# Kernel tuning notes

Hardware: AMD Instinct MI355X
Metric: run time of the kernel (lower is better)

## Reference

```python
import jax, jax.numpy as jnp
import numpy as np

# dims: batch, seq, d_model, d_hidden, routed experts, top-k, shared experts
B, S, D, H, E_R, K, E_S = 2, 1024, 1024, 512, 64, 6, 2
EPS = 1.1920929e-07  # torch.finfo(float32).eps, RMSNorm default when eps=None


def setup_inputs() -> dict:
    key = jax.random.key(0)
    ks = jax.random.split(key, 8)
    u = lambda k, shape, b: jax.random.uniform(k, shape, jnp.float32, -b, b)
    bd = 1.0 / np.sqrt(D)   # bound for W1 (1/sqrt(d_input)) and W2 (1/sqrt(d_output)=1/sqrt(D))
    bh = 1.0 / np.sqrt(H)
    return {
        "x": jax.random.normal(ks[0], (B, S, D), jnp.float32),
        "norm_w": jnp.ones((D,), jnp.float32),            # RMSNorm weight
        "Wr": u(ks[1], (E_R, D), bd),                      # router Linear weight (no bias)
        "sW1": u(ks[2], (E_S, D, H), bd), "sb1": jnp.zeros((E_S, 1, H), jnp.float32),
        "sW2": u(ks[3], (E_S, H, D), bd), "sb2": jnp.zeros((E_S, 1, D), jnp.float32),
        "sWg": u(ks[4], (H, H), bh),                       # shared-experts SwiGLU gate weight
        "rW1": u(ks[5], (E_R, D, H), bd), "rb1": jnp.zeros((E_R, 1, H), jnp.float32),
        "rW2": u(ks[6], (E_R, H, D), bd), "rb2": jnp.zeros((E_R, 1, D), jnp.float32),
        "rWg": u(ks[7], (H, H), bh),                       # routed-experts SwiGLU gate weight
        "bias": jnp.full((E_R,), 1.0 / E_R, jnp.float32), # routing bias buffer (expert_bias=True)
    }


def _rmsnorm(x, w):
    ms = jnp.mean(x * x, axis=-1, keepdims=True)
    return x * jax.lax.rsqrt(ms + EPS) * w


def _swiglu(h, Wg):
    # SwiGLU(d_model=H): silu(h @ Wg) * h, elementwise gate over hidden dim
    return jax.nn.silu(h @ Wg) * h


def reference(x, norm_w, Wr, sW1, sb1, sW2, sb2, sWg, rW1, rb1, rW2, rb2, rWg, bias):
    xn = _rmsnorm(x, norm_w)
    t = xn.reshape(-1, D)                                  # (T, D) tokens
    # --- shared experts, summed over expert axis ---
    hs = jnp.einsum('td,edh->teh', t, sW1) + sb1[None, :, 0, :]
    hs = _swiglu(hs, sWg)
    shared = jnp.einsum('teh,ehd->td', hs, sW2) + jnp.sum(sb2[:, 0, :], axis=0)
    # --- router ---
    raw = t @ Wr.T                                         # (T, E_R) raw affinity
    aff = jax.lax.stop_gradient(raw) + bias                # detached + bias for top-k selection
    _, idx = jax.lax.top_k(aff, K)                         # (T, K)
    # --- routed experts: dense all-expert FFN, gather top-k outputs ---
    # (mathematically identical to the source's per-token weight gather,
    #  but avoids materializing (T,K,D,H) weight tensors)
    h = jnp.einsum('td,edh->teh', t, rW1) + rb1[None, :, 0, :]   # (T, E_R, H)
    h = _swiglu(h, rWg)
    out_all = jnp.einsum('teh,ehd->ted', h, rW2) + rb2[None, :, 0, :]  # (T, E_R, D)
    out_k = jnp.take_along_axis(out_all, idx[:, :, None], axis=1)      # (T, K, D)
    aff_k = jnp.take_along_axis(raw, idx, axis=1)                      # (T, K) raw (undetached)
    w = aff_k / jnp.sum(aff_k, axis=-1, keepdims=True)                 # expert_bias=True path
    routed = jnp.einsum('tk,tkd->td', w, out_k)                        # (T, D)
    return x + (shared + routed).reshape(B, S, D)
```

## Files before the change

kernel.cpp:

```cpp
#include <hip/hip_runtime.h>
#include <cstdint>
#include <cstddef>

typedef unsigned short u16;
typedef unsigned int u32;
typedef __attribute__((ext_vector_type(8))) short bh8;
typedef __attribute__((ext_vector_type(4))) float fx4;

#define T_TOK 2048
#define D_DIM 1024
#define H_DIM 512
#define N_EXP 64
#define K_TOP 6
#define N_ASG (T_TOK * K_TOP)
#define R_TOT (N_ASG + 2 * T_TOK)
#define GRID_E (8 * 9 * 64)

__device__ __forceinline__ float bf2f(u16 v) {
    union { u32 u; float f; } c; c.u = ((u32)v) << 16; return c.f;
}
__device__ __forceinline__ u16 f2bf(float f) {
    union { u32 u; float f; } c; c.f = f;
    u32 u = c.u;
    return (u16)((u + 0x7fffu + ((u >> 16) & 1u)) >> 16);
}

__global__ __launch_bounds__(256) void rn4_k(
    const float* __restrict__ x, const float* __restrict__ nw,
    const float* __restrict__ Wr, float* __restrict__ raw, u16* __restrict__ xnb)
{
    int t0 = blockIdx.x << 2, tid = threadIdx.x;
    __shared__ float xs[4][D_DIM];
    __shared__ float ps[4][256];
    __shared__ float red4[4][4];
    int d0 = tid << 2;
    float4 wv = *(const float4*)(nw + d0);
    float4 xv[4];
    #pragma unroll
    for (int tt = 0; tt < 4; ++tt) {
        xv[tt] = *(const float4*)(x + (size_t)(t0 + tt) * D_DIM + d0);
        float ss = xv[tt].x * xv[tt].x + xv[tt].y * xv[tt].y
                 + xv[tt].z * xv[tt].z + xv[tt].w * xv[tt].w;
        #pragma unroll
        for (int o = 32; o > 0; o >>= 1) ss += __shfl_down(ss, o);
        if ((tid & 63) == 0) red4[tt][tid >> 6] = ss;
    }
    __syncthreads();
    #pragma unroll
    for (int tt = 0; tt < 4; ++tt) {
        float ms = (red4[tt][0] + red4[tt][1] + red4[tt][2] + red4[tt][3]) * (1.f / (float)D_DIM);
        float sc = rsqrtf(ms + 1.1920929e-07f);
        float4 xf;
        xf.x = xv[tt].x * sc * wv.x;
        xf.y = xv[tt].y * sc * wv.y;
        xf.z = xv[tt].z * sc * wv.z;
        xf.w = xv[tt].w * sc * wv.w;
        *(float4*)&xs[tt][d0] = xf;
        ushort4 ob;
        ob.x = f2bf(xf.x); ob.y = f2bf(xf.y); ob.z = f2bf(xf.z); ob.w = f2bf(xf.w);
        *(ushort4*)(xnb + (size_t)(t0 + tt) * D_DIM + d0) = ob;
    }
    __syncthreads();
    int e = tid & 63, part = tid >> 6;
    const float* wr = Wr + (size_t)e * D_DIM + part * 256;
    float s0 = 0.f, s1 = 0.f, s2 = 0.f, s3 = 0.f;
    const float* xp0 = &xs[0][part * 256];
    const float* xp1 = &xs[1][part * 256];
    const float* xp2 = &xs[2][part * 256];
    const float* xp3 = &xs[3][part * 256];
    #pragma unroll 4
    for (int i = 0; i < 256; i += 4) {
        float4 w4 = *(const float4*)(wr + i);
        s0 += xp0[i] * w4.x + xp0[i+1] * w4.y + xp0[i+2] * w4.z + xp0[i+3] * w4.w;
        s1 += xp1[i] * w4.x + xp1[i+1] * w4.y + xp1[i+2] * w4.z + xp1[i+3] * w4.w;
        s2 += xp2[i] * w4.x + xp2[i+1] * w4.y + xp2[i+2] * w4.z + xp2[i+3] * w4.w;
        s3 += xp3[i] * w4.x + xp3[i+1] * w4.y + xp3[i+2] * w4.z + xp3[i+3] * w4.w;
    }
    ps[0][tid] = s0; ps[1][tid] = s1; ps[2][tid] = s2; ps[3][tid] = s3;
    __syncthreads();
    if (part == 0) {
        #pragma unroll
        for (int tt = 0; tt < 4; ++tt)
            raw[(size_t)(t0 + tt) * N_EXP + e] =
                ps[tt][e] + ps[tt][64 + e] + ps[tt][128 + e] + ps[tt][192 + e];
    }
}

__global__ void topk_k(const float* __restrict__ raw, const float* __restrict__ ebias,
                       int* __restrict__ cnt, int* __restrict__ tki, float* __restrict__ tkw)
{
    int t = blockIdx.x, lane = threadIdx.x;
    float r = raw[(size_t)t * N_EXP + lane];
    float cur = r + ebias[lane];
    int selI[K_TOP]; float selR[K_TOP];
    #pragma unroll
    for (int k = 0; k < K_TOP; ++k) {
        float v = cur; int id = lane;
        #pragma unroll
        for (int o = 32; o > 0; o >>= 1) {
            float v2 = __shfl_down(v, o); int i2 = __shfl_down(id, o);
            if (v2 > v || (v2 == v && i2 < id)) { v = v2; id = i2; }
        }
        id = __shfl(id, 0);
        if (lane == id) cur = -3.4e38f;
        selI[k] = id;
        selR[k] = __shfl(r, id);
    }
    float s = 0.f;
    #pragma unroll
    for (int k = 0; k < K_TOP; ++k) s += selR[k];
    if (lane < K_TOP) {
        tki[t * K_TOP + lane] = selI[lane];
        tkw[t * K_TOP + lane] = selR[lane] / s;
        atomicAdd(&cnt[selI[lane]], 1);
    }
}

__global__ void scan_k(const int* __restrict__ cnt, int* __restrict__ offs, int* __restrict__ fill)
{
    int lane = threadIdx.x;
    int c = cnt[lane];
    int s = c;
    #pragma unroll
    for (int o = 1; o < 64; o <<= 1) {
        int v = __shfl_up(s, o);
        if (lane >= o) s += v;
    }
    int excl = s - c;
    offs[lane] = excl;
    fill[lane] = excl;
    if (lane == 63) offs[N_EXP] = s;
}

__global__ void fill_k(const int* __restrict__ tki, const float* __restrict__ tkw,
                       int* __restrict__ fill, int* __restrict__ atok, float* __restrict__ aw,
                       int* __restrict__ rowOf)
{
    int t = blockIdx.x, lane = threadIdx.x;
    if (lane < K_TOP) {
        int e = tki[t * K_TOP + lane];
        int p = atomicAdd(&fill[e], 1);
        atok[p] = t;
        aw[p] = tkw[t * K_TOP + lane];
        rowOf[t * K_TOP + lane] = p;
    }
}

__global__ __launch_bounds__(256) void convAll_k(
    const float* __restrict__ rW1, const float* __restrict__ sW1,
    const float* __restrict__ rW2, const float* __restrict__ sW2,
    const float* __restrict__ rWg, const float* __restrict__ sWg,
    u16* __restrict__ W1f, u16* __restrict__ W2f, u16* __restrict__ Wgf)
{
    int id = blockIdx.x;
    const float* src; u16* dst;
    int K, N, n0, k0;
    const size_t MS = (size_t)H_DIM * D_DIM;
    if (id < 66 * 128) {
        int mat = id >> 7, tile = id & 127;
        K = D_DIM; N = H_DIM;
        src = (mat < N_EXP ? rW1 + (size_t)mat * MS : sW1 + (size_t)(mat - N_EXP) * MS);
        dst = W1f + (size_t)mat * MS;
        n0 = (tile & 7) << 6; k0 = (tile >> 3) << 6;
    } else if (id < 2 * 66 * 128) {
        id -= 66 * 128;
        int mat = id >> 7, tile = id & 127;
        K = H_DIM; N = D_DIM;
        src = (mat < N_EXP ? rW2 + (size_t)mat * MS : sW2 + (size_t)(mat - N_EXP) * MS);
        dst = W2f + (size_t)mat * MS;
        n0 = (tile & 15) << 6; k0 = (tile >> 4) << 6;
    } else {
        id -= 2 * 66 * 128;
        int mat = id >> 6, tile = id & 63;
        K = H_DIM; N = H_DIM;
        src = (mat == 0 ? rWg : sWg);
        dst = Wgf + (size_t)mat * (H_DIM * H_DIM);
        n0 = (tile & 7) << 6; k0 = (tile >> 3) << 6;
    }

    __shared__ u16 t[64][68];
    int tid = threadIdx.x;
    int kr = tid >> 4, c4 = (tid & 15) << 2;
    #pragma unroll
    for (int rr = 0; rr < 4; ++rr) {
        int k = (rr << 4) + kr;
        float4 v = *(const float4*)(src + (size_t)(k0 + k) * N + n0 + c4);
        t[c4 + 0][k] = f2bf(v.x);
        t[c4 + 1][k] = f2bf(v.y);
        t[c4 + 2][k] = f2bf(v.z);
        t[c4 + 3][k] = f2bf(v.w);
    }
    __syncthreads();
    int lane = tid & 63, g = tid >> 6;
    int nr = lane & 15, kq = lane >> 4;
    #pragma unroll
    for (int f = 0; f < 2; ++f) {
        int fragId = g + (f << 2);
        int ntile = fragId >> 1, kb = fragId & 1;
        bh8 v = *(const bh8*)&t[(ntile << 4) + nr][(kb << 5) + (kq << 3)];
        size_t fi = (((size_t)((n0 >> 4) + ntile) * (size_t)(K >> 5)
                      + (size_t)((k0 >> 5) + kb)) << 9) + (size_t)(lane << 3);
        *(bh8*)(dst + fi) = v;
    }
}

__device__ __forceinline__ bool slabDecode(
    int bx, const int* __restrict__ offs,
    int& e, int& rowBase, int& rows, int& tokBase)
{
    int xcd = bx & 7, rest = bx >> 3, grp = rest >> 6, slab = rest & 63;
    if (grp < 8) {
        e = (grp << 3) + xcd;
        int s0 = offs[e], s1 = offs[e + 1];
        rowBase = s0 + (slab << 5);
        if (rowBase >= s1) return false;
        rows = s1 - rowBase; if (rows > 32) rows = 32;
        tokBase = -1;
        return true;
    }
    int f = (slab << 3) + xcd;
    if (f >= 128) return false;
    int sh = f & 1;
    e = N_EXP + sh;
    tokBase = (f >> 1) << 5;
    rowBase = N_ASG + (sh << 11) + tokBase;
    rows = 32;
    return true;
}

__global__ __launch_bounds__(256, 4) void p1_k(
    const u16* __restrict__ xnb, const u16* __restrict__ W1f,
    const float* __restrict__ rb1, const float* __restrict__ sb1,
    const int* __restrict__ offs, const int* __restrict__ atok,
    u16* __restrict__ h)
{
    int e, rowBase, rows, tokBase;
    if (!slabDecode(blockIdx.x, offs, e, rowBase, rows, tokBase)) return;

    __shared__ int tok[32];
    int tid = threadIdx.x;
    if (tid < 32) {
        int cl = tid < rows ? tid : rows - 1;
        tok[tid] = (tokBase < 0) ? atok[rowBase + cl] : tokBase + tid;
    }
    __syncthreads();

    int w = tid >> 6, lane = tid & 63, quad = lane >> 4, l15 = lane & 15;
    int cg = blockIdx.y;
    int nt0 = (cg << 4) + (w << 2);
    const u16* bp = W1f + (size_t)e * (H_DIM * D_DIM)
                  + (((size_t)nt0 << 5) << 9) + (lane << 3);
    const u16* a0p = xnb + (size_t)tok[l15] * D_DIM + (quad << 3);
    const u16* a1p = xnb + (size_t)tok[16 + l15] * D_DIM + (quad << 3);
    const float* b1 = (tokBase < 0) ? rb1 + e * H_DIM : sb1 + (e - N_EXP) * H_DIM;

    fx4 ac0[4] = {}, ac1[4] = {};
    bh8 bA[4], bB[4], aA0, aA1, aB0, aB1;
    #pragma unroll
    for (int ct = 0; ct < 4; ++ct) bA[ct] = *(const bh8*)(bp + ((size_t)(ct << 5) << 9));
    aA0 = *(const bh8*)a0p; aA1 = *(const bh8*)a1p;
    #pragma unroll 1
    for (int kb = 0; kb < 32; kb += 2) {
        #pragma unroll
        for (int ct = 0; ct < 4; ++ct) bB[ct] = *(const bh8*)(bp + (((ct << 5) + kb + 1) << 9));
        aB0 = *(const bh8*)(a0p + ((kb + 1) << 5));
        aB1 = *(const bh8*)(a1p + ((kb + 1) << 5));
        #pragma unroll
        for (int ct = 0; ct < 4; ++ct) {
            ac0[ct] = __builtin_amdgcn_mfma_f32_16x16x32_bf16(aA0, bA[ct], ac0[ct], 0, 0, 0);
            ac1[ct] = __builtin_amdgcn_mfma_f32_16x16x32_bf16(aA1, bA[ct], ac1[ct], 0, 0, 0);
        }
        #pragma unroll
        for (int ct = 0; ct < 4; ++ct) bA[ct] = *(const bh8*)(bp + (((ct << 5) + kb + 2) << 9));
        aA0 = *(const bh8*)(a0p + ((kb + 2) << 5));
        aA1 = *(const bh8*)(a1p + ((kb + 2) << 5));
        #pragma unroll
        for (int ct = 0; ct < 4; ++ct) {
            ac0[ct] = __builtin_amdgcn_mfma_f32_16x16x32_bf16(aB0, bB[ct], ac0[ct], 0, 0, 0);
            ac1[ct] = __builtin_amdgcn_mfma_f32_16x16x32_bf16(aB1, bB[ct], ac1[ct], 0, 0, 0);
        }
    }
    #pragma unroll
    for (int ct = 0; ct < 4; ++ct) {
        int col = ((nt0 + ct) << 4) + l15;
        float bv = b1[col];
        #pragma unroll
        for (int r = 0; r < 4; ++r) {
            int r0 = (quad << 2) + r;
            if (r0 < rows) h[(size_t)(rowBase + r0) * H_DIM + col] = f2bf(ac0[ct][r] + bv);
            int r1 = 16 + r0;
            if (r1 < rows) h[(size_t)(rowBase + r1) * H_DIM + col] = f2bf(ac1[ct][r] + bv);
        }
    }
}

__global__ __launch_bounds__(256, 4) void p2_k(
    u16* __restrict__ h, const u16* __restrict__ Wgf)
{
    int rowBase = blockIdx.x << 4;
    int tid = threadIdx.x;
    int w = tid >> 6, lane = tid & 63, quad = lane >> 4, l15 = lane & 15;
    const u16* bp = Wgf + (rowBase < N_ASG ? 0 : (size_t)(H_DIM * H_DIM)) + (lane << 3);
    const u16* a0p = h + (size_t)(rowBase + l15) * H_DIM + (quad << 3);

    fx4 ac[8] = {};
    bh8 bA[8], bB[8], aA, aB;
    #pragma unroll
    for (int ct = 0; ct < 8; ++ct)
        bA[ct] = *(const bh8*)(bp + ((((size_t)(w << 3) + ct) << 4) << 9));
    aA = *(const bh8*)a0p;
    #pragma unroll 1
    for (int kb = 0; kb < 16; kb += 2) {
        #pragma unroll
        for (int ct = 0; ct < 8; ++ct)
            bB[ct] = *(const bh8*)(bp + (((((size_t)(w << 3) + ct) << 4) + kb + 1) << 9));
        aB = *(const bh8*)(a0p + ((kb + 1) << 5));
        #pragma unroll
        for (int ct = 0; ct < 8; ++ct)
            ac[ct] = __builtin_amdgcn_mfma_f32_16x16x32_bf16(aA, bA[ct], ac[ct], 0, 0, 0);
        #pragma unroll
        for (int ct = 0; ct < 8; ++ct)
            bA[ct] = *(const bh8*)(bp + (((((size_t)(w << 3) + ct) << 4) + kb + 2) << 9));
        aA = *(const bh8*)(a0p + ((kb + 2) << 5));
        #pragma unroll
        for (int ct = 0; ct < 8; ++ct)
            ac[ct] = __builtin_amdgcn_mfma_f32_16x16x32_bf16(aB, bB[ct], ac[ct], 0, 0, 0);
    }
    __syncthreads();
    #pragma unroll
    for (int ct = 0; ct < 8; ++ct) {
        int col = (((w << 3) + ct) << 4) + l15;
        #pragma unroll
        for (int r = 0; r < 4; ++r) {
            int row = rowBase + (quad << 2) + r;
            size_t i = (size_t)row * H_DIM + col;
            float g = ac[ct][r], hv = bf2f(h[i]);
            h[i] = f2bf(hv * g * (1.f / (1.f + __expf(-g))));
        }
    }
}

template<int ATOM>
__global__ __launch_bounds__(256, 4) void p3_k(
    const u16* __restrict__ hg, const u16* __restrict__ W2f,
    const float* __restrict__ rb2, const float* __restrict__ sb2,
    const int* __restrict__ offs, const int* __restrict__ atok,
    const float* __restrict__ aw, float* __restrict__ accG, float* __restrict__ outAll)
{
    int e, rowBase, rows, tokBase;
    if (!slabDecode(blockIdx.x, offs, e, rowBase, rows, tokBase)) return;

    __shared__ int tok[32];
    __shared__ float wt[32];
    int tid = threadIdx.x;
    if (tid < 32) {
        int cl = tid < rows ? tid : rows - 1;
        if (tokBase < 0) { tok[tid] = atok[rowBase + cl]; wt[tid] = aw[rowBase + cl]; }
        else             { tok[tid] = tokBase + tid;      wt[tid] = 1.0f; }
    }
    __syncthreads();

    int w = tid >> 6, lane = tid & 63, quad = lane >> 4, l15 = lane & 15;
    int cg = blockIdx.y;
    int nt0 = (cg << 4) + (w << 2);
    const u16* bp = W2f + (size_t)e * (H_DIM * D_DIM)
                  + (((size_t)nt0 << 4) << 9) + (lane << 3);
    const u16* a0p = hg + (size_t)(rowBase + l15) * H_DIM + (quad << 3);
    const u16* a1p = hg + (size_t)(rowBase + 16 + l15) * H_DIM + (quad << 3);
    const float* b2 = (tokBase < 0) ? rb2 + e * D_DIM : sb2 + (e - N_EXP) * D_DIM;

    fx4 ac0[4] = {}, ac1[4] = {};
    bh8 bA[4], bB[4], aA0, aA1, aB0, aB1;
    #pragma unroll
    for (int ct = 0; ct < 4; ++ct) bA[ct] = *(const bh8*)(bp + ((size_t)(ct << 4) << 9));
    aA0 = *(const bh8*)a0p; aA1 = *(const bh8*)a1p;
    #pragma unroll 1
    for (int kb = 0; kb < 16; kb += 2) {
        #pragma unroll
        for (int ct = 0; ct < 4; ++ct) bB[ct] = *(const bh8*)(bp + (((ct << 4) + kb + 1) << 9));
        aB0 = *(const bh8*)(a0p + ((kb + 1) << 5));
        aB1 = *(const bh8*)(a1p + ((kb + 1) << 5));
        #pragma unroll
        for (int ct = 0; ct < 4; ++ct) {
            ac0[ct] = __builtin_amdgcn_mfma_f32_16x16x32_bf16(aA0, bA[ct], ac0[ct], 0, 0, 0);
            ac1[ct] = __builtin_amdgcn_mfma_f32_16x16x32_bf16(aA1, bA[ct], ac1[ct], 0, 0, 0);
        }
        #pragma unroll
        for (int ct = 0; ct < 4; ++ct) bA[ct] = *(const bh8*)(bp + (((ct << 4) + kb + 2) << 9));
        aA0 = *(const bh8*)(a0p + ((kb + 2) << 5));
        aA1 = *(const bh8*)(a1p + ((kb + 2) << 5));
        #pragma unroll
        for (int ct = 0; ct < 4; ++ct) {
            ac0[ct] = __builtin_amdgcn_mfma_f32_16x16x32_bf16(aB0, bB[ct], ac0[ct], 0, 0, 0);
            ac1[ct] = __builtin_amdgcn_mfma_f32_16x16x32_bf16(aB1, bB[ct], ac1[ct], 0, 0, 0);
        }
    }
    #pragma unroll
    for (int ct = 0; ct < 4; ++ct) {
        int col = ((nt0 + ct) << 4) + l15;
        float bv = b2[col];
        #pragma unroll
        for (int r = 0; r < 4; ++r) {
            int r0 = (quad << 2) + r;
            if (r0 < rows) {
                float v = wt[r0] * (ac0[ct][r] + bv);
                if (ATOM) atomicAdd(&accG[(size_t)tok[r0] * D_DIM + col], v);
                else      outAll[(size_t)(rowBase + r0) * D_DIM + col] = v;
            }
            int r1 = 16 + r0;
            if (r1 < rows) {
                float v = wt[r1] * (ac1[ct][r] + bv);
                if (ATOM) atomicAdd(&accG[(size_t)tok[r1] * D_DIM + col], v);
                else      outAll[(size_t)(rowBase + r1) * D_DIM + col] = v;
            }
        }
    }
}

__global__ __launch_bounds__(256) void gather_k(
    const float* __restrict__ x, const float* __restrict__ outAll,
    const int* __restrict__ rowOf, float* __restrict__ out)
{
    int t = blockIdx.x, tid = threadIdx.x;
    __shared__ int rws[K_TOP];
    if (tid < K_TOP) rws[tid] = rowOf[t * K_TOP + tid];
    __syncthreads();
    int d0 = tid << 2;
    size_t base = (size_t)t * D_DIM + d0;
    float4 xv = *(const float4*)(x + base);
    float4 s = *(const float4*)(outAll + (size_t)(N_ASG + t) * D_DIM + d0);
    float4 s1 = *(const float4*)(outAll + (size_t)(N_ASG + T_TOK + t) * D_DIM + d0);
    s.x += s1.x; s.y += s1.y; s.z += s1.z; s.w += s1.w;
    #pragma unroll
    for (int k = 0; k < K_TOP; ++k) {
        float4 v = *(const float4*)(outAll + (size_t)rws[k] * D_DIM + d0);
        s.x += v.x; s.y += v.y; s.z += v.z; s.w += v.w;
    }
    float4 o;
    o.x = xv.x + s.x; o.y = xv.y + s.y; o.z = xv.z + s.z; o.w = xv.w + s.w;
    *(float4*)(out + base) = o;
}

template<int ROUTED>
__global__ __launch_bounds__(256) void moe_ffn_k(
    const u16* __restrict__ xnb,
    const float* __restrict__ W1b, const float* __restrict__ Wg,
    const float* __restrict__ W2b,
    const float* __restrict__ b1b, const float* __restrict__ b2b,
    const int* __restrict__ offs, const int* __restrict__ atok,
    const float* __restrict__ aw, float* __restrict__ accG)
{
    int e = blockIdx.z;
    int start = ROUTED ? offs[e] : 0;
    int end   = ROUTED ? offs[e + 1] : T_TOK;
    int rowBase = start + (blockIdx.y << 5);
    if (rowBase >= end) return;
    int rows = end - rowBase; if (rows > 32) rows = 32;

    __shared__ int   tok[32];
    __shared__ float wt[32];
    __shared__ u16 hA[32 * 520];
    __shared__ u16 hG[32 * 520];
    __shared__ u16 As[32 * 32];
    __shared__ u16 Bs[64 * 36];

    int tid = threadIdx.x;
    if (tid < 32) {
        int cl = rowBase + tid; if (cl >= end) cl = end - 1;
        tok[tid] = ROUTED ? atok[cl] : cl;
        wt[tid]  = ROUTED ? aw[cl] : 1.0f;
    }
    __syncthreads();

    const float* W1 = W1b + (size_t)e * (D_DIM * H_DIM);
    const float* W2 = W2b + (size_t)e * (D_DIM * H_DIM);
    const float* b1 = b1b + e * H_DIM;
    const float* b2 = b2b + e * D_DIM;

    int w = tid >> 6, lane = tid & 63, quad = lane >> 4, l15 = lane & 15;
    int sr2 = tid >> 3, sc2 = (tid & 7) << 2;

    for (int nc = 0; nc < 8; ++nc) {
        int n0 = nc << 6;
        fx4 a0 = {}; fx4 a1 = {};
        for (int kc = 0; kc < 32; ++kc) {
            int kb = kc << 5;
            int2 av = *(const int2*)(xnb + (size_t)tok[sr2] * D_DIM + kb + sc2);
            const float* cp = W1 + n0 + lane;
            int kx = kb + (w << 3);
            u32 p[4];
            #pragma unroll
            for (int jj = 0; jj < 4; ++jj) {
                u32 lo = f2bf(cp[(size_t)(kx + 2 * jj) * H_DIM]);
                u32 hi = f2bf(cp[(size_t)(kx + 2 * jj + 1) * H_DIM]);
                p[jj] = lo | (hi << 16);
            }
            __syncthreads();
            *(int2*)&As[sr2 * 32 + sc2] = av;
            u16* bsw = &Bs[lane * 36 + (w << 3)];
            uint2 q0; q0.x = p[0]; q0.y = p[1];
            uint2 q1; q1.x = p[2]; q1.y = p[3];
            *(uint2*)bsw = q0;
            *(uint2*)(bsw + 4) = q1;
            __syncthreads();
            bh8 af0 = *(const bh8*)&As[l15 * 32 + (quad << 3)];
            bh8 af1 = *(const bh8*)&As[(16 + l15) * 32 + (quad << 3)];
            const u16* brp = &Bs[((w << 4) + l15) * 36 + (quad << 3)];
            union { bh8 v; uint2 u2[2]; } bf;
            bf.u2[0] = *(const uint2*)brp;
            bf.u2[1] = *(const uint2*)(brp + 4);
            a0 = __builtin_amdgcn_mfma_f32_16x16x32_bf16(af0, bf.v, a0, 0, 0, 0);
            a1 = __builtin_amdgcn_mfma_f32_16x16x32_bf16(af1, bf.v, a1, 0, 0, 0);
        }
        int col = n0 + (w << 4) + l15;
        float bv = b1[col];
        #pragma unroll
        for (int r = 0; r < 4; ++r) {
            hA[((quad << 2) + r) * 520 + col]      = f2bf(a0[r] + bv);
            hA[(16 + (quad << 2) + r) * 520 + col] = f2bf(a1[r] + bv);
        }
    }
    __syncthreads();

    for (int nc = 0; nc < 8; ++nc) {
        int n0 = nc << 6;
        fx4 a0 = {}; fx4 a1 = {};
        for (int kc = 0; kc < 16; ++kc) {
            int kb = kc << 5;
            const float* cp = Wg + n0 + lane;
            int kx = kb + (w << 3);
            u32 p[4];
            #pragma unroll
            for (int jj = 0; jj < 4; ++jj) {
                u32 lo = f2bf(cp[(size_t)(kx + 2 * jj) * H_DIM]);
                u32 hi = f2bf(cp[(size_t)(kx + 2 * jj + 1) * H_DIM]);
                p[jj] = lo | (hi << 16);
            }
            __syncthreads();
            u16* bsw = &Bs[lane * 36 + (w << 3)];
            uint2 q0; q0.x = p[0]; q0.y = p[1];
            uint2 q1; q1.x = p[2]; q1.y = p[3];
            *(uint2*)bsw = q0;
            *(uint2*)(bsw + 4) = q1;
            __syncthreads();
            bh8 af0 = *(const bh8*)&hA[l15 * 520 + kb + (quad << 3)];
            bh8 af1 = *(const bh8*)&hA[(16 + l15) * 520 + kb + (quad << 3)];
            const u16* brp = &Bs[((w << 4) + l15) * 36 + (quad << 3)];
            union { bh8 v; uint2 u2[2]; } bf;
            bf.u2[0] = *(const uint2*)brp;
            bf.u2[1] = *(const uint2*)(brp + 4);
            a0 = __builtin_amdgcn_mfma_f32_16x16x32_bf16(af0, bf.v, a0, 0, 0, 0);
            a1 = __builtin_amdgcn_mfma_f32_16x16x32_bf16(af1, bf.v, a1, 0, 0, 0);
        }
        int col = n0 + (w << 4) + l15;
        #pragma unroll
        for (int r = 0; r < 4; ++r) {
            int r0 = (quad << 2) + r;
            float h0 = bf2f(hA[r0 * 520 + col]);
            float g0 = a0[r];
            hG[r0 * 520 + col] = f2bf(h0 * g0 * (1.f / (1.f + __expf(-g0))));
            int r1 = 16 + r0;
            float h1 = bf2f(hA[r1 * 520 + col]);
            float g1 = a1[r];
            hG[r1 * 520 + col] = f2bf(h1 * g1 * (1.f / (1.f + __expf(-g1))));
        }
    }
    __syncthreads();

    for (int nc = 0; nc < 16; ++nc) {
        int n0 = nc << 6;
        fx4 a0 = {}; fx4 a1 = {};
        for (int kc = 0; kc < 16; ++kc) {
            int kb = kc << 5;
            const float* cp = W2 + n0 + lane;
            int kx = kb + (w << 3);
            u32 p[4];
            #pragma unroll
            for (int jj = 0; jj < 4; ++jj) {
                u32 lo = f2bf(cp[(size_t)(kx + 2 * jj) * D_DIM]);
                u32 hi = f2bf(cp[(size_t)(kx + 2 * jj + 1) * D_DIM]);
                p[jj] = lo | (hi << 16);
            }
            __syncthreads();
            u16* bsw = &Bs[lane * 36 + (w << 3)];
            uint2 q0; q0.x = p[0]; q0.y = p[1];
            uint2 q1; q1.x = p[2]; q1.y = p[3];
            *(uint2*)bsw = q0;
            *(uint2*)(bsw + 4) = q1;
            __syncthreads();
            bh8 af0 = *(const bh8*)&hG[l15 * 520 + kb + (quad << 3)];
            bh8 af1 = *(const bh8*)&hG[(16 + l15) * 520 + kb + (quad << 3)];
            const u16* brp = &Bs[((w << 4) + l15) * 36 + (quad << 3)];
            union { bh8 v; uint2 u2[2]; } bf;
            bf.u2[0] = *(const uint2*)brp;
            bf.u2[1] = *(const uint2*)(brp + 4);
            a0 = __builtin_amdgcn_mfma_f32_16x16x32_bf16(af0, bf.v, a0, 0, 0, 0);
            a1 = __builtin_amdgcn_mfma_f32_16x16x32_bf16(af1, bf.v, a1, 0, 0, 0);
        }
        int col = n0 + (w << 4) + l15;
        float bv = b2[col];
        #pragma unroll
        for (int r = 0; r < 4; ++r) {
            int lr0 = (quad << 2) + r;
            if (lr0 < rows)
                atomicAdd(&accG[(size_t)tok[lr0] * D_DIM + col], wt[lr0] * (a0[r] + bv));
            int lr1 = 16 + lr0;
            if (lr1 < rows)
                atomicAdd(&accG[(size_t)tok[lr1] * D_DIM + col], wt[lr1] * (a1[r] + bv));
        }
    }
}

__global__ __launch_bounds__(256) void final_k(
    const float* __restrict__ x, const float* __restrict__ acc, float* __restrict__ out)
{
    size_t i = ((size_t)blockIdx.x * 256 + threadIdx.x) << 2;
    float4 xv = *(const float4*)(x + i);
    float4 a = *(const float4*)(acc + i);
    float4 o;
    o.x = xv.x + a.x;
    o.y = xv.y + a.y;
    o.z = xv.z + a.z;
    o.w = xv.w + a.w;
    *(float4*)(out + i) = o;
}

extern "C" void kernel_launch(void* const* d_in, const int* in_sizes, int n_in,
                              void* d_out, int out_size, void* d_ws, size_t ws_size,
                              hipStream_t stream)
{
    const float* x     = (const float*)d_in[0];
    const float* nw    = (const float*)d_in[1];
    const float* Wr    = (const float*)d_in[2];
    const float* sW1   = (const float*)d_in[3];
    const float* sb1   = (const float*)d_in[4];
    const float* sW2   = (const float*)d_in[5];
    const float* sb2   = (const float*)d_in[6];
    const float* sWg   = (const float*)d_in[7];
    const float* rW1   = (const float*)d_in[8];
    const float* rb1   = (const float*)d_in[9];
    const float* rW2   = (const float*)d_in[10];
    const float* rb2   = (const float*)d_in[11];
    const float* rWg   = (const float*)d_in[12];
    const float* ebias = (const float*)d_in[13];
    float* out = (float*)d_out;
    (void)in_sizes; (void)n_in; (void)out_size;

    char* wp = (char*)d_ws;
    auto alloc = [&](size_t b) { char* p = wp; wp += (b + 255) & ~(size_t)255; return p; };
    int*   cnt  = (int*)alloc(N_EXP * 4);
    int*   offs = (int*)alloc((N_EXP + 1) * 4);
    int*   fill = (int*)alloc(N_EXP * 4);
    int*   tki  = (int*)alloc((size_t)T_TOK * K_TOP * 4);
    float* tkw  = (float*)alloc((size_t)T_TOK * K_TOP * 4);
    int*   atok = (int*)alloc((size_t)N_ASG * 4);
    float* aw   = (float*)alloc((size_t)N_ASG * 4);
    int*   rowOf= (int*)alloc((size_t)T_TOK * K_TOP * 4);
    float* raw  = (float*)alloc((size_t)T_TOK * N_EXP * 4);
    u16*   xnb  = (u16*)alloc((size_t)T_TOK * D_DIM * 2);
    float* acc  = (float*)alloc((size_t)T_TOK * D_DIM * 4);
    u16* W1f = (u16*)alloc((size_t)(N_EXP + 2) * H_DIM * D_DIM * 2);
    u16* W2f = (u16*)alloc((size_t)(N_EXP + 2) * H_DIM * D_DIM * 2);
    u16* Wgf = (u16*)alloc((size_t)2 * H_DIM * H_DIM * 2);
    u16* h   = (u16*)alloc((size_t)R_TOT * H_DIM * 2);
    alloc(1 << 16);
    char* markA = wp;
    float* outAll = (float*)alloc((size_t)R_TOT * D_DIM * 4);
    char* markB = wp;
    bool fastA = (size_t)(markA - (char*)d_ws) <= ws_size;
    bool fast2 = (size_t)(markB - (char*)d_ws) <= ws_size;

    hipMemsetAsync(cnt, 0, N_EXP * 4, stream);

    dim3 b256(256);
    rn4_k<<<T_TOK / 4, b256, 0, stream>>>(x, nw, Wr, raw, xnb);
    topk_k<<<T_TOK, dim3(64), 0, stream>>>(raw, ebias, cnt, tki, tkw);
    scan_k<<<1, dim3(64), 0, stream>>>(cnt, offs, fill);
    fill_k<<<T_TOK, dim3(64), 0, stream>>>(tki, tkw, fill, atok, aw, rowOf);

    if (fast2) {
        convAll_k<<<dim3(2 * 66 * 128 + 2 * 64), b256, 0, stream>>>(
            rW1, sW1, rW2, sW2, rWg, sWg, W1f, W2f, Wgf);
        p1_k<<<dim3(GRID_E, 2), b256, 0, stream>>>(xnb, W1f, rb1, sb1, offs, atok, h);
        p2_k<<<dim3(R_TOT / 16), b256, 0, stream>>>(h, Wgf);
        p3_k<0><<<dim3(GRID_E, 4), b256, 0, stream>>>(
            h, W2f, rb2, sb2, offs, atok, aw, nullptr, outAll);
        gather_k<<<T_TOK, b256, 0, stream>>>(x, outAll, rowOf, out);
    } else if (fastA) {
        hipMemsetAsync(acc, 0, (size_t)T_TOK * D_DIM * 4, stream);
        convAll_k<<<dim3(2 * 66 * 128 + 2 * 64), b256, 0, stream>>>(
            rW1, sW1, rW2, sW2, rWg, sWg, W1f, W2f, Wgf);
        p1_k<<<dim3(GRID_E, 2), b256, 0, stream>>>(xnb, W1f, rb1, sb1, offs, atok, h);
        p2_k<<<dim3(R_TOT / 16), b256, 0, stream>>>(h, Wgf);
        p3_k<1><<<dim3(GRID_E, 4), b256, 0, stream>>>(
            h, W2f, rb2, sb2, offs, atok, aw, acc, nullptr);
        final_k<<<(T_TOK * D_DIM) / 1024, b256, 0, stream>>>(x, acc, out);
    } else {
        hipMemsetAsync(acc, 0, (size_t)T_TOK * D_DIM * 4, stream);
        moe_ffn_k<1><<<dim3(1, 64, N_EXP), b256, 0, stream>>>(
            xnb, rW1, rWg, rW2, rb1, rb2, offs, atok, aw, acc);
        moe_ffn_k<0><<<dim3(1, 64, 2), b256, 0, stream>>>(
            xnb, sW1, sWg, sW2, sb1, sb2, offs, atok, aw, acc);
        final_k<<<(T_TOK * D_DIM) / 1024, b256, 0, stream>>>(x, acc, out);
    }
}
```

Baseline: 638.6 us.

## Fuse weight conversion into prep kernel and stage GEMM epilogues through LDS

Merges the bf16 weight-conversion pass into the RMSNorm/router kernel so both run in a single launch, with each conversion block now covering two 64-row k-slabs and prefetching the second slab while the first is written out. The p1 and p3 (non-atomic) epilogues now stage results in shared memory and write them to global memory as contiguous 16-byte row segments, replacing scattered per-element stores. This is meant to cut launch overhead and uncoalesced write traffic. In exchange it uses more LDS per block, which may lower occupancy, and adds an extra barrier in the epilogues.

```diff
diff --git a/kernel.cpp b/kernel.cpp
--- a/kernel.cpp
+++ b/kernel.cpp
@@ -15,6 +15,7 @@
 #define N_ASG (T_TOK * K_TOP)
 #define R_TOT (N_ASG + 2 * T_TOK)
 #define GRID_E (8 * 9 * 64)
+#define NCONV (66 * 64 + 66 * 64 + 64)
 
 __device__ __forceinline__ float bf2f(u16 v) {
     union { u32 u; float f; } c; c.u = ((u32)v) << 16; return c.f;
@@ -25,49 +26,134 @@
     return (u16)((u + 0x7fffu + ((u >> 16) & 1u)) >> 16);
 }
 
-__global__ __launch_bounds__(256) void rn4_k(
+__global__ __launch_bounds__(256) void prep_k(
     const float* __restrict__ x, const float* __restrict__ nw,
-    const float* __restrict__ Wr, float* __restrict__ raw, u16* __restrict__ xnb)
-{
-    int t0 = blockIdx.x << 2, tid = threadIdx.x;
-    __shared__ float xs[4][D_DIM];
-    __shared__ float ps[4][256];
-    __shared__ float red4[4][4];
+    const float* __restrict__ Wr, float* __restrict__ raw, u16* __restrict__ xnb,
+    const float* __restrict__ rW1, const float* __restrict__ sW1,
+    const float* __restrict__ rW2, const float* __restrict__ sW2,
+    const float* __restrict__ rWg, const float* __restrict__ sWg,
+    u16* __restrict__ W1f, u16* __restrict__ W2f, u16* __restrict__ Wgf,
+    int nconv)
+{
+    __shared__ __align__(16) char smraw[20608];
+    int id = blockIdx.x;
+    int tid = threadIdx.x;
+
+    if (id < nconv) {
+        const size_t MS = (size_t)H_DIM * D_DIM;
+        const float* src; u16* dst;
+        int K, N, n0, k0;
+        if (id < 4224) {
+            int mat = id >> 6, j = id & 63;
+            K = D_DIM; N = H_DIM;
+            src = (mat < N_EXP ? rW1 + (size_t)mat * MS : sW1 + (size_t)(mat - N_EXP) * MS);
+            dst = W1f + (size_t)mat * MS;
+            n0 = (j & 7) << 6; k0 = (j >> 3) << 7;
+        } else if (id < 8448) {
+            int t = id - 4224, mat = t >> 6, j = t & 63;
+            K = H_DIM; N = D_DIM;
+            src = (mat < N_EXP ? rW2 + (size_t)mat * MS : sW2 + (size_t)(mat - N_EXP) * MS);
+            dst = W2f + (size_t)mat * MS;
+            n0 = (j & 15) << 6; k0 = (j >> 4) << 7;
+        } else {
+            int t = id - 8448, mat = t >> 5, j = t & 31;
+            K = H_DIM; N = H_DIM;
+            src = (mat == 0 ? rWg : sWg);
+            dst = Wgf + (size_t)mat * (H_DIM * H_DIM);
+            n0 = (j & 7) << 6; k0 = (j >> 3) << 7;
+        }
+        u16 (*t0)[68] = reinterpret_cast<u16(*)[68]>(smraw);
+        u16 (*t1)[68] = reinterpret_cast<u16(*)[68]>(smraw + 8704);
+        int kr = tid >> 4, c4 = (tid & 15) << 2;
+        int lane = tid & 63, g = tid >> 6, nr = lane & 15, kq = lane >> 4;
+
+        float4 v[4];
+        #pragma unroll
+        for (int rr = 0; rr < 4; ++rr)
+            v[rr] = *(const float4*)(src + (size_t)(k0 + (rr << 4) + kr) * N + n0 + c4);
+        #pragma unroll
+        for (int rr = 0; rr < 4; ++rr) {
+            int k = (rr << 4) + kr;
+            t0[c4 + 0][k] = f2bf(v[rr].x);
+            t0[c4 + 1][k] = f2bf(v[rr].y);
+            t0[c4 + 2][k] = f2bf(v[rr].z);
+            t0[c4 + 3][k] = f2bf(v[rr].w);
+        }
+        __syncthreads();
+        float4 w4_[4];
+        #pragma unroll
+        for (int rr = 0; rr < 4; ++rr)
+            w4_[rr] = *(const float4*)(src + (size_t)(k0 + 64 + (rr << 4) + kr) * N + n0 + c4);
+        #pragma unroll
+        for (int f = 0; f < 2; ++f) {
+            int fragId = g + (f << 2);
+            int ntile = fragId >> 1, kb2 = fragId & 1;
+            bh8 vv = *(const bh8*)&t0[(ntile << 4) + nr][(kb2 << 5) + (kq << 3)];
+            size_t fi = (((size_t)((n0 >> 4) + ntile) * (size_t)(K >> 5)
+                          + (size_t)((k0 >> 5) + kb2)) << 9) + (size_t)(lane << 3);
+            *(bh8*)(dst + fi) = vv;
+        }
+        #pragma unroll
+        for (int rr = 0; rr < 4; ++rr) {
+            int k = (rr << 4) + kr;
+            t1[c4 + 0][k] = f2bf(w4_[rr].x);
+            t1[c4 + 1][k] = f2bf(w4_[rr].y);
+            t1[c4 + 2][k] = f2bf(w4_[rr].z);
+            t1[c4 + 3][k] = f2bf(w4_[rr].w);
+        }
+        __syncthreads();
+        #pragma unroll
+        for (int f = 0; f < 2; ++f) {
+            int fragId = g + (f << 2);
+            int ntile = fragId >> 1, kb2 = fragId & 1;
+            bh8 vv = *(const bh8*)&t1[(ntile << 4) + nr][(kb2 << 5) + (kq << 3)];
+            size_t fi = (((size_t)((n0 >> 4) + ntile) * (size_t)(K >> 5)
+                          + (size_t)((k0 >> 5) + 2 + kb2)) << 9) + (size_t)(lane << 3);
+            *(bh8*)(dst + fi) = vv;
+        }
+        return;
+    }
+
+    int t0tok = (id - nconv) << 2;
+    float* xs = (float*)smraw;
+    float* ps = xs + 4 * D_DIM;
+    float* red4 = ps + 4 * 256;
     int d0 = tid << 2;
     float4 wv = *(const float4*)(nw + d0);
     float4 xv[4];
     #pragma unroll
     for (int tt = 0; tt < 4; ++tt) {
-        xv[tt] = *(const float4*)(x + (size_t)(t0 + tt) * D_DIM + d0);
+        xv[tt] = *(const float4*)(x + (size_t)(t0tok + tt) * D_DIM + d0);
         float ss = xv[tt].x * xv[tt].x + xv[tt].y * xv[tt].y
                  + xv[tt].z * xv[tt].z + xv[tt].w * xv[tt].w;
         #pragma unroll
         for (int o = 32; o > 0; o >>= 1) ss += __shfl_down(ss, o);
-        if ((tid & 63) == 0) red4[tt][tid >> 6] = ss;
+        if ((tid & 63) == 0) red4[tt * 4 + (tid >> 6)] = ss;
     }
     __syncthreads();
     #pragma unroll
     for (int tt = 0; tt < 4; ++tt) {
-        float ms = (red4[tt][0] + red4[tt][1] + red4[tt][2] + red4[tt][3]) * (1.f / (float)D_DIM);
+        float ms = (red4[tt * 4 + 0] + red4[tt * 4 + 1] + red4[tt * 4 + 2] + red4[tt * 4 + 3])
+                 * (1.f / (float)D_DIM);
         float sc = rsqrtf(ms + 1.1920929e-07f);
         float4 xf;
         xf.x = xv[tt].x * sc * wv.x;
         xf.y = xv[tt].y * sc * wv.y;
         xf.z = xv[tt].z * sc * wv.z;
         xf.w = xv[tt].w * sc * wv.w;
-        *(float4*)&xs[tt][d0] = xf;
+        *(float4*)&xs[tt * D_DIM + d0] = xf;
         ushort4 ob;
         ob.x = f2bf(xf.x); ob.y = f2bf(xf.y); ob.z = f2bf(xf.z); ob.w = f2bf(xf.w);
-        *(ushort4*)(xnb + (size_t)(t0 + tt) * D_DIM + d0) = ob;
+        *(ushort4*)(xnb + (size_t)(t0tok + tt) * D_DIM + d0) = ob;
     }
     __syncthreads();
     int e = tid & 63, part = tid >> 6;
     const float* wr = Wr + (size_t)e * D_DIM + part * 256;
     float s0 = 0.f, s1 = 0.f, s2 = 0.f, s3 = 0.f;
-    const float* xp0 = &xs[0][part * 256];
-    const float* xp1 = &xs[1][part * 256];
-    const float* xp2 = &xs[2][part * 256];
-    const float* xp3 = &xs[3][part * 256];
+    const float* xp0 = &xs[0 * D_DIM + part * 256];
+    const float* xp1 = &xs[1 * D_DIM + part * 256];
+    const float* xp2 = &xs[2 * D_DIM + part * 256];
+    const float* xp3 = &xs[3 * D_DIM + part * 256];
     #pragma unroll 4
     for (int i = 0; i < 256; i += 4) {
         float4 w4 = *(const float4*)(wr + i);
@@ -76,13 +162,15 @@
         s2 += xp2[i] * w4.x + xp2[i+1] * w4.y + xp2[i+2] * w4.z + xp2[i+3] * w4.w;
         s3 += xp3[i] * w4.x + xp3[i+1] * w4.y + xp3[i+2] * w4.z + xp3[i+3] * w4.w;
     }
-    ps[0][tid] = s0; ps[1][tid] = s1; ps[2][tid] = s2; ps[3][tid] = s3;
+    ps[0 * 256 + tid] = s0; ps[1 * 256 + tid] = s1;
+    ps[2 * 256 + tid] = s2; ps[3 * 256 + tid] = s3;
     __syncthreads();
     if (part == 0) {
         #pragma unroll
         for (int tt = 0; tt < 4; ++tt)
-            raw[(size_t)(t0 + tt) * N_EXP + e] =
-                ps[tt][e] + ps[tt][64 + e] + ps[tt][128 + e] + ps[tt][192 + e];
+            raw[(size_t)(t0tok + tt) * N_EXP + e] =
+                ps[tt * 256 + e] + ps[tt * 256 + 64 + e]
+              + ps[tt * 256 + 128 + e] + ps[tt * 256 + 192 + e];
     }
 }
 
@@ -143,64 +231,6 @@
         atok[p] = t;
         aw[p] = tkw[t * K_TOP + lane];
         rowOf[t * K_TOP + lane] = p;
-    }
-}
-
-__global__ __launch_bounds__(256) void convAll_k(
-    const float* __restrict__ rW1, const float* __restrict__ sW1,
-    const float* __restrict__ rW2, const float* __restrict__ sW2,
-    const float* __restrict__ rWg, const float* __restrict__ sWg,
-    u16* __restrict__ W1f, u16* __restrict__ W2f, u16* __restrict__ Wgf)
-{
-    int id = blockIdx.x;
-    const float* src; u16* dst;
-    int K, N, n0, k0;
-    const size_t MS = (size_t)H_DIM * D_DIM;
-    if (id < 66 * 128) {
-        int mat = id >> 7, tile = id & 127;
-        K = D_DIM; N = H_DIM;
-        src = (mat < N_EXP ? rW1 + (size_t)mat * MS : sW1 + (size_t)(mat - N_EXP) * MS);
-        dst = W1f + (size_t)mat * MS;
-        n0 = (tile & 7) << 6; k0 = (tile >> 3) << 6;
-    } else if (id < 2 * 66 * 128) {
-        id -= 66 * 128;
-        int mat = id >> 7, tile = id & 127;
-        K = H_DIM; N = D_DIM;
-        src = (mat < N_EXP ? rW2 + (size_t)mat * MS : sW2 + (size_t)(mat - N_EXP) * MS);
-        dst = W2f + (size_t)mat * MS;
-        n0 = (tile & 15) << 6; k0 = (tile >> 4) << 6;
-    } else {
-        id -= 2 * 66 * 128;
-        int mat = id >> 6, tile = id & 63;
-        K = H_DIM; N = H_DIM;
-        src = (mat == 0 ? rWg : sWg);
-        dst = Wgf + (size_t)mat * (H_DIM * H_DIM);
-        n0 = (tile & 7) << 6; k0 = (tile >> 3) << 6;
-    }
-
-    __shared__ u16 t[64][68];
-    int tid = threadIdx.x;
-    int kr = tid >> 4, c4 = (tid & 15) << 2;
-    #pragma unroll
-    for (int rr = 0; rr < 4; ++rr) {
-        int k = (rr << 4) + kr;
-        float4 v = *(const float4*)(src + (size_t)(k0 + k) * N + n0 + c4);
-        t[c4 + 0][k] = f2bf(v.x);
-        t[c4 + 1][k] = f2bf(v.y);
-        t[c4 + 2][k] = f2bf(v.z);
-        t[c4 + 3][k] = f2bf(v.w);
-    }
-    __syncthreads();
-    int lane = tid & 63, g = tid >> 6;
-    int nr = lane & 15, kq = lane >> 4;
-    #pragma unroll
-    for (int f = 0; f < 2; ++f) {
-        int fragId = g + (f << 2);
-        int ntile = fragId >> 1, kb = fragId & 1;
-        bh8 v = *(const bh8*)&t[(ntile << 4) + nr][(kb << 5) + (kq << 3)];
-        size_t fi = (((size_t)((n0 >> 4) + ntile) * (size_t)(K >> 5)
-                      + (size_t)((k0 >> 5) + kb)) << 9) + (size_t)(lane << 3);
-        *(bh8*)(dst + fi) = v;
     }
 }
 
@@ -238,6 +268,7 @@
     if (!slabDecode(blockIdx.x, offs, e, rowBase, rows, tokBase)) return;
 
     __shared__ int tok[32];
+    __shared__ u16 hs[32][264];
     int tid = threadIdx.x;
     if (tid < 32) {
         int cl = tid < rows ? tid : rows - 1;
@@ -282,15 +313,22 @@
     }
     #pragma unroll
     for (int ct = 0; ct < 4; ++ct) {
-        int col = ((nt0 + ct) << 4) + l15;
-        float bv = b1[col];
+        int lcol = (((w << 2) + ct) << 4) + l15;
+        float bv = b1[(cg << 8) + lcol];
         #pragma unroll
         for (int r = 0; r < 4; ++r) {
             int r0 = (quad << 2) + r;
-            if (r0 < rows) h[(size_t)(rowBase + r0) * H_DIM + col] = f2bf(ac0[ct][r] + bv);
-            int r1 = 16 + r0;
-            if (r1 < rows) h[(size_t)(rowBase + r1) * H_DIM + col] = f2bf(ac1[ct][r] + bv);
-        }
+            hs[r0][lcol]      = f2bf(ac0[ct][r] + bv);
+            hs[16 + r0][lcol] = f2bf(ac1[ct][r] + bv);
+        }
+    }
+    __syncthreads();
+    #pragma unroll
+    for (int p = 0; p < 4; ++p) {
+        int idx = tid + (p << 8);
+        int r = idx >> 5, cs = (idx & 31) << 3;
+        if (r < rows)
+            *(uint4*)&h[(size_t)(rowBase + r) * H_DIM + (cg << 8) + cs] = *(uint4*)&hs[r][cs];
     }
 }
 
@@ -352,6 +390,7 @@
 
     __shared__ int tok[32];
     __shared__ float wt[32];
+    __shared__ float os[ATOM ? 1 : 32 * 260];
     int tid = threadIdx.x;
     if (tid < 32) {
         int cl = tid < rows ? tid : rows - 1;
@@ -395,24 +434,41 @@
             ac1[ct] = __builtin_amdgcn_mfma_f32_16x16x32_bf16(aB1, bB[ct], ac1[ct], 0, 0, 0);
         }
     }
-    #pragma unroll
-    for (int ct = 0; ct < 4; ++ct) {
-        int col = ((nt0 + ct) << 4) + l15;
-        float bv = b2[col];
-        #pragma unroll
-        for (int r = 0; r < 4; ++r) {
-            int r0 = (quad << 2) + r;
-            if (r0 < rows) {
-                float v = wt[r0] * (ac0[ct][r] + bv);
-                if (ATOM) atomicAdd(&accG[(size_t)tok[r0] * D_DIM + col], v);
-                else      outAll[(size_t)(rowBase + r0) * D_DIM + col] = v;
+    if (ATOM) {
+        #pragma unroll
+        for (int ct = 0; ct < 4; ++ct) {
+            int col = ((nt0 + ct) << 4) + l15;
+            float bv = b2[col];
+            #pragma unroll
+            for (int r = 0; r < 4; ++r) {
+                int r0 = (quad << 2) + r;
+                if (r0 < rows)
+                    atomicAdd(&accG[(size_t)tok[r0] * D_DIM + col], wt[r0] * (ac0[ct][r] + bv));
+                int r1 = 16 + r0;
+                if (r1 < rows)
+                    atomicAdd(&accG[(size_t)tok[r1] * D_DIM + col], wt[r1] * (ac1[ct][r] + bv));
             }
-            int r1 = 16 + r0;
-            if (r1 < rows) {
-                float v = wt[r1] * (ac1[ct][r] + bv);
-                if (ATOM) atomicAdd(&accG[(size_t)tok[r1] * D_DIM + col], v);
-                else      outAll[(size_t)(rowBase + r1) * D_DIM + col] = v;
+        }
+    } else {
+        #pragma unroll
+        for (int ct = 0; ct < 4; ++ct) {
+            int lcol = (((w << 2) + ct) << 4) + l15;
+            float bv = b2[(cg << 8) + lcol];
+            #pragma unroll
+            for (int r = 0; r < 4; ++r) {
+                int r0 = (quad << 2) + r;
+                os[r0 * 260 + lcol]        = wt[r0] * (ac0[ct][r] + bv);
+                os[(16 + r0) * 260 + lcol] = wt[16 + r0] * (ac1[ct][r] + bv);
             }
+        }
+        __syncthreads();
+        #pragma unroll
+        for (int p = 0; p < 8; ++p) {
+            int idx = tid + (p << 8);
+            int r = idx >> 6, cs = (idx & 63) << 2;
+            if (r < rows)
+                *(float4*)&outAll[(size_t)(rowBase + r) * D_DIM + (cg << 8) + cs]
+                    = *(float4*)&os[r * 260 + cs];
         }
     }
 }
@@ -673,14 +729,19 @@
     hipMemsetAsync(cnt, 0, N_EXP * 4, stream);
 
     dim3 b256(256);
-    rn4_k<<<T_TOK / 4, b256, 0, stream>>>(x, nw, Wr, raw, xnb);
+    if (fast2 || fastA) {
+        prep_k<<<dim3(NCONV + T_TOK / 4), b256, 0, stream>>>(
+            x, nw, Wr, raw, xnb, rW1, sW1, rW2, sW2, rWg, sWg, W1f, W2f, Wgf, NCONV);
+    } else {
+        prep_k<<<dim3(T_TOK / 4), b256, 0, stream>>>(
+            x, nw, Wr, raw, xnb, rW1, sW1, rW2, sW2, rWg, sWg,
+            nullptr, nullptr, nullptr, 0);
+    }
     topk_k<<<T_TOK, dim3(64), 0, stream>>>(raw, ebias, cnt, tki, tkw);
     scan_k<<<1, dim3(64), 0, stream>>>(cnt, offs, fill);
     fill_k<<<T_TOK, dim3(64), 0, stream>>>(tki, tkw, fill, atok, aw, rowOf);
 
     if (fast2) {
-        convAll_k<<<dim3(2 * 66 * 128 + 2 * 64), b256, 0, stream>>>(
-            rW1, sW1, rW2, sW2, rWg, sWg, W1f, W2f, Wgf);
         p1_k<<<dim3(GRID_E, 2), b256, 0, stream>>>(xnb, W1f, rb1, sb1, offs, atok, h);
         p2_k<<<dim3(R_TOT / 16), b256, 0, stream>>>(h, Wgf);
         p3_k<0><<<dim3(GRID_E, 4), b256, 0, stream>>>(
@@ -688,8 +749,6 @@
         gather_k<<<T_TOK, b256, 0, stream>>>(x, outAll, rowOf, out);
     } else if (fastA) {
         hipMemsetAsync(acc, 0, (size_t)T_TOK * D_DIM * 4, stream);
-        convAll_k<<<dim3(2 * 66 * 128 + 2 * 64), b256, 0, stream>>>(
-            rW1, sW1, rW2, sW2, rWg, sWg, W1f, W2f, Wgf);
         p1_k<<<dim3(GRID_E, 2), b256, 0, stream>>>(xnb, W1f, rb1, sb1, offs, atok, h);
         p2_k<<<dim3(R_TOT / 16), b256, 0, stream>>>(h, Wgf);
         p3_k<1><<<dim3(GRID_E, 4), b256, 0, stream>>>(
```

Result: no change. 631.3 us (-1.2%).
